# Optimization experiments

Measured on AMD Instinct MI355X. Metric: run time of the kernel, lower is better.

## Reference

```python
import jax, jax.numpy as jnp
import numpy as np

KH, KW = 3, 3  # spatial kernel from kernel_size=(1,3,3,C)


def _extract_patches_valid(x, kh, kw):
    # TF extract_image_patches ordering: depth = (row, col, channel) flattened.
    B, H, W, C = x.shape
    Ho, Wo = H - kh + 1, W - kw + 1
    # stack kh*kw shifted views -> [B, Ho, Wo, kh*kw, C]
    views = [x[:, i:i + Ho, j:j + Wo, :] for i in range(kh) for j in range(kw)]
    patches = jnp.stack(views, axis=3)
    return patches.reshape(B, Ho, Wo, kh * kw * C)


def setup_inputs() -> dict:
    key = jax.random.key(0)
    k1, k2, k3 = jax.random.split(key, 3)
    B, H, W, C = 32, 112, 112, 32
    filters = 128
    patch_dim = KH * KW * C  # 288
    x = jax.random.normal(k1, (B, H, W, C), dtype=jnp.float32)
    ccs = jax.random.uniform(k2, (patch_dim, filters), dtype=jnp.float32)  # RandomUniform(0,1)
    beta = jax.random.uniform(k3, (filters,), dtype=jnp.float32)
    return {"x": x, "ccs": ccs, "beta": beta}


def reference(x, ccs, beta):
    B = x.shape[0]
    patch_dim, filters = ccs.shape
    patches = _extract_patches_valid(x, KH, KW)  # [B, Ho, Wo, patch_dim]
    Ho, Wo = patches.shape[1], patches.shape[2]
    p = patches.reshape(B, Ho * Wo, patch_dim)  # [B, P, D]
    # squared distance: ||p||^2 - 2 p.ccs + ||ccs||^2  -> [B, P, filters]
    p_sq = jnp.sum(p * p, axis=2, keepdims=True)
    c_sq = jnp.sum(ccs * ccs, axis=0, keepdims=True)
    scores = p_sq - 2.0 * jnp.einsum('bpd,df->bpf', p, ccs) + c_sq
    out = jnp.exp(-beta * scores)  # RBF activation, beta broadcast over filters
    return out.reshape(B, Ho, Wo, filters)
```

## Files before the change

kernel.cpp:

```cpp
#include <hip/hip_runtime.h>


typedef __attribute__((ext_vector_type(8))) short bf16x8;
typedef __attribute__((ext_vector_type(4))) float f32x4;

#define HH 112
#define WW 112
#define CC 32
#define HO 110
#define WO 110
#define NF 128
#define KD 288
#define RPX 114
#define XP 32
#define ORPB 2
#define SROWS 4

__device__ __forceinline__ unsigned short f32_to_bf16(float f) {
    unsigned u = __float_as_uint(f);
    unsigned r = u + 0x7FFFu + ((u >> 16) & 1u);
    return (unsigned short)(r >> 16);
}

__global__ __launch_bounds__(256) void rbf_prologue(const float* __restrict__ ccs,
                                                    unsigned short* __restrict__ ccs_t,
                                                    float* __restrict__ c_sq) {
    int idx = blockIdx.x * 256 + threadIdx.x;
    int d = idx >> 7;
    int f = idx & 127;
    ccs_t[f * KD + d] = f32_to_bf16(ccs[idx]);
    if (blockIdx.x == 0 && threadIdx.x < 128) {
        const int fc = threadIdx.x;
        float s = 0.f;
        #pragma unroll 8
        for (int dd = 0; dd < KD; ++dd) {
            float v = ccs[dd * NF + fc];
            s += v * v;
        }
        c_sq[fc] = s;
    }
}

__global__ __launch_bounds__(256, 4) void rbf_main(const float* __restrict__ x,
                                                   const unsigned short* __restrict__ ccs_t,
                                                   const float* __restrict__ c_sq,
                                                   const float* __restrict__ beta,
                                                   float* __restrict__ out) {
    __shared__ unsigned short xs[SROWS * RPX * XP];
    __shared__ float colsum[452];
    __shared__ float p_sq[ORPB * 112];

    const int t = threadIdx.x;
    const int y0 = blockIdx.x * ORPB;
    const int b = blockIdx.y;

    #pragma unroll
    for (int p = 0; p < 14; ++p) {
        int idx = t + p * 256;
        int q = idx & 7;
        int ic = idx >> 3;
        int col = ic % 112;
        int i = ic / 112;
        const float4 v = *(const float4*)(x + ((size_t)(b * HH + y0 + i) * WW + col) * CC + q * 4);
        unsigned short h0 = f32_to_bf16(v.x), h1 = f32_to_bf16(v.y);
        unsigned short h2 = f32_to_bf16(v.z), h3 = f32_to_bf16(v.w);
        uint2 pk;
        pk.x = (unsigned)h0 | ((unsigned)h1 << 16);
        pk.y = (unsigned)h2 | ((unsigned)h3 << 16);
        *(uint2*)(&xs[(i * RPX + col) * XP + q * 4]) = pk;
        float part = v.x * v.x + v.y * v.y + v.z * v.z + v.w * v.w;
        part += __shfl_xor(part, 1);
        part += __shfl_xor(part, 2);
        part += __shfl_xor(part, 4);
        if (q == 0) colsum[ic] = part;
    }
    __syncthreads();

    if (t < ORPB * 112) {
        int r = t / 112;
        int c = t - r * 112;
        float s = 0.f;
        #pragma unroll
        for (int i = 0; i < 3; ++i)
            #pragma unroll
            for (int j = 0; j < 3; ++j)
                s += colsum[(r + i) * 112 + c + j];
        p_sq[t] = s;
    }
    __syncthreads();

    const int lane  = t & 63;
    const int wave  = t >> 6;
    const int laneM = lane & 15;
    const int quad  = lane >> 4;
    const int pl    = laneM & 1;

    const unsigned short* ap0 = ccs_t + (size_t)(wave * 32 + laneM) * KD + quad * 8;
    const unsigned short* ap1 = ap0 + 16 * KD;

    const int fb = wave * 32 + quad * 4;

    for (int r = 0; r < ORPB; ++r) {
        f32x4 acc[7][2];
        #pragma unroll
        for (int mi = 0; mi < 7; ++mi) {
            acc[mi][0] = (f32x4){0.f, 0.f, 0.f, 0.f};
            acc[mi][1] = (f32x4){0.f, 0.f, 0.f, 0.f};
        }

        #pragma unroll
        for (int kb = 0; kb < 9; ++kb) {
            const int ki = kb / 3, kj = kb % 3;
            bf16x8 a0 = *(const bf16x8*)(ap0 + kb * 32);
            bf16x8 a1 = *(const bf16x8*)(ap1 + kb * 32);
            #pragma unroll
            for (int mi = 0; mi < 7; ++mi) {
                const bf16x8 bf = *(const bf16x8*)(&xs[((r + ki) * RPX + mi * 16 + laneM + kj) * XP + quad * 8]);
                acc[mi][0] = __builtin_amdgcn_mfma_f32_16x16x32_bf16(a0, bf, acc[mi][0], 0, 0, 0);
                acc[mi][1] = __builtin_amdgcn_mfma_f32_16x16x32_bf16(a1, bf, acc[mi][1], 0, 0, 0);
            }
        }

        const float4 cs0 = *(const float4*)(c_sq + fb);
        const float4 cs1 = *(const float4*)(c_sq + fb + 16);
        const float4 bt0 = *(const float4*)(beta + fb);
        const float4 bt1 = *(const float4*)(beta + fb + 16);
        float* orow = out + (size_t)((b * HO + y0 + r) * WO) * NF;
        #pragma unroll
        for (int mi = 0; mi < 7; ++mi) {
            const int px = mi * 16 + laneM;
            const float ps = p_sq[r * 112 + px];
            f32x4 o0, o1;
            o0[0] = __expf(-bt0.x * (ps - 2.f * acc[mi][0][0] + cs0.x));
            o0[1] = __expf(-bt0.y * (ps - 2.f * acc[mi][0][1] + cs0.y));
            o0[2] = __expf(-bt0.z * (ps - 2.f * acc[mi][0][2] + cs0.z));
            o0[3] = __expf(-bt0.w * (ps - 2.f * acc[mi][0][3] + cs0.w));
            o1[0] = __expf(-bt1.x * (ps - 2.f * acc[mi][1][0] + cs1.x));
            o1[1] = __expf(-bt1.y * (ps - 2.f * acc[mi][1][1] + cs1.y));
            o1[2] = __expf(-bt1.z * (ps - 2.f * acc[mi][1][2] + cs1.z));
            o1[3] = __expf(-bt1.w * (ps - 2.f * acc[mi][1][3] + cs1.w));

            f32x4 sendv = pl ? o0 : o1;
            f32x4 recv;
            recv[0] = __shfl_xor(sendv[0], 1);
            recv[1] = __shfl_xor(sendv[1], 1);
            recv[2] = __shfl_xor(sendv[2], 1);
            recv[3] = __shfl_xor(sendv[3], 1);
            const f32x4 v1 = pl ? recv : o0;
            const f32x4 v2 = pl ? o1 : recv;

            const int pxe = mi * 16 + (laneM & ~1);
            float* op1 = orow + (size_t)pxe * NF + fb + pl * 16;
            if (pxe < WO)
                __builtin_nontemporal_store(v1, (f32x4*)op1);
            if (pxe + 1 < WO)
                __builtin_nontemporal_store(v2, (f32x4*)(op1 + NF));
        }
    }
}

extern "C" void kernel_launch(void* const* d_in, const int* in_sizes, int n_in,
                              void* d_out, int out_size, void* d_ws, size_t ws_size,
                              hipStream_t stream) {
    const float* x    = (const float*)d_in[0];
    const float* ccs  = (const float*)d_in[1];
    const float* beta = (const float*)d_in[2];
    float* out = (float*)d_out;

    unsigned short* ccs_t = (unsigned short*)d_ws;
    float* c_sq = (float*)((char*)d_ws + 128 * KD * sizeof(unsigned short));

    rbf_prologue<<<144, 256, 0, stream>>>(ccs, ccs_t, c_sq);
    rbf_main<<<dim3(55, 32), 256, 0, stream>>>(x, ccs_t, c_sq, beta, out);
}
```

Baseline: 262.3 us.

## Process eight output rows per block with rolling smem ring and prefetch

```diff
diff --git a/kernel.cpp b/kernel.cpp
--- a/kernel.cpp
+++ b/kernel.cpp
@@ -13,8 +13,8 @@
 #define KD 288
 #define RPX 114
 #define XP 32
-#define ORPB 2
-#define SROWS 4
+#define SLOTS 6
+#define CSP 116
 
 __device__ __forceinline__ unsigned short f32_to_bf16(float f) {
     unsigned u = __float_as_uint(f);
@@ -41,18 +41,25 @@
     }
 }
 
-__global__ __launch_bounds__(256, 4) void rbf_main(const float* __restrict__ x,
-                                                   const unsigned short* __restrict__ ccs_t,
-                                                   const float* __restrict__ c_sq,
-                                                   const float* __restrict__ beta,
-                                                   float* __restrict__ out) {
-    __shared__ unsigned short xs[SROWS * RPX * XP];
-    __shared__ float colsum[452];
-    __shared__ float p_sq[ORPB * 112];
+__global__ __launch_bounds__(256) void rbf_main(const float* __restrict__ x,
+                                                const unsigned short* __restrict__ ccs_t,
+                                                const float* __restrict__ c_sq,
+                                                const float* __restrict__ beta,
+                                                float* __restrict__ out) {
+    __shared__ unsigned short xs[SLOTS * RPX * XP];
+    __shared__ float colsum[SLOTS * CSP];
+    __shared__ float p_sq[2 * 112];
 
     const int t = threadIdx.x;
-    const int y0 = blockIdx.x * ORPB;
-    const int b = blockIdx.y;
+    const int y0 = blockIdx.x * 8;
+    const int b  = blockIdx.y;
+    const int ns = (HO - y0 >= 8) ? 4 : ((HO - y0) >> 1);
+
+    const int lane  = t & 63;
+    const int wave  = t >> 6;
+    const int laneM = lane & 15;
+    const int quad  = lane >> 4;
+    const int pl    = laneM & 1;
 
     #pragma unroll
     for (int p = 0; p < 14; ++p) {
@@ -72,89 +79,145 @@
         part += __shfl_xor(part, 1);
         part += __shfl_xor(part, 2);
         part += __shfl_xor(part, 4);
-        if (q == 0) colsum[ic] = part;
+        if (q == 0) colsum[i * CSP + col] = part;
     }
     __syncthreads();
 
-    if (t < ORPB * 112) {
-        int r = t / 112;
-        int c = t - r * 112;
+    if (t < 224) {
+        int r = t / 112, c = t - (t / 112) * 112;
         float s = 0.f;
         #pragma unroll
         for (int i = 0; i < 3; ++i)
             #pragma unroll
             for (int j = 0; j < 3; ++j)
-                s += colsum[(r + i) * 112 + c + j];
+                s += colsum[(r + i) * CSP + c + j];
         p_sq[t] = s;
     }
     __syncthreads();
-
-    const int lane  = t & 63;
-    const int wave  = t >> 6;
-    const int laneM = lane & 15;
-    const int quad  = lane >> 4;
-    const int pl    = laneM & 1;
 
     const unsigned short* ap0 = ccs_t + (size_t)(wave * 32 + laneM) * KD + quad * 8;
     const unsigned short* ap1 = ap0 + 16 * KD;
 
     const int fb = wave * 32 + quad * 4;
-
-    for (int r = 0; r < ORPB; ++r) {
-        f32x4 acc[7][2];
+    const float4 cs0 = *(const float4*)(c_sq + fb);
+    const float4 cs1 = *(const float4*)(c_sq + fb + 16);
+    const float4 bt0 = *(const float4*)(beta + fb);
+    const float4 bt1 = *(const float4*)(beta + fb + 16);
+
+    float4 pre[7];
+
+    for (int k = 0; k < ns; ++k) {
+        const bool more = (k < ns - 1);
+
+        if (more) {
+            #pragma unroll
+            for (int p = 0; p < 7; ++p) {
+                int idx = t + p * 256;
+                int ic = idx >> 3;
+                int q = idx & 7;
+                int col = ic % 112;
+                int i = ic / 112;
+                pre[p] = *(const float4*)(x + ((size_t)(b * HH + y0 + 2 * k + 4 + i) * WW + col) * CC + q * 4);
+            }
+        }
+
+        int sb[4];
         #pragma unroll
-        for (int mi = 0; mi < 7; ++mi) {
-            acc[mi][0] = (f32x4){0.f, 0.f, 0.f, 0.f};
-            acc[mi][1] = (f32x4){0.f, 0.f, 0.f, 0.f};
-        }
-
-        #pragma unroll
-        for (int kb = 0; kb < 9; ++kb) {
-            const int ki = kb / 3, kj = kb % 3;
-            bf16x8 a0 = *(const bf16x8*)(ap0 + kb * 32);
-            bf16x8 a1 = *(const bf16x8*)(ap1 + kb * 32);
+        for (int d = 0; d < 4; ++d) sb[d] = ((2 * k + d) % SLOTS) * RPX;
+
+        for (int r = 0; r < 2; ++r) {
+            f32x4 acc[7][2];
             #pragma unroll
             for (int mi = 0; mi < 7; ++mi) {
-                const bf16x8 bf = *(const bf16x8*)(&xs[((r + ki) * RPX + mi * 16 + laneM + kj) * XP + quad * 8]);
-                acc[mi][0] = __builtin_amdgcn_mfma_f32_16x16x32_bf16(a0, bf, acc[mi][0], 0, 0, 0);
-                acc[mi][1] = __builtin_amdgcn_mfma_f32_16x16x32_bf16(a1, bf, acc[mi][1], 0, 0, 0);
-            }
-        }
-
-        const float4 cs0 = *(const float4*)(c_sq + fb);
-        const float4 cs1 = *(const float4*)(c_sq + fb + 16);
-        const float4 bt0 = *(const float4*)(beta + fb);
-        const float4 bt1 = *(const float4*)(beta + fb + 16);
-        float* orow = out + (size_t)((b * HO + y0 + r) * WO) * NF;
-        #pragma unroll
-        for (int mi = 0; mi < 7; ++mi) {
-            const int px = mi * 16 + laneM;
-            const float ps = p_sq[r * 112 + px];
-            f32x4 o0, o1;
-            o0[0] = __expf(-bt0.x * (ps - 2.f * acc[mi][0][0] + cs0.x));
-            o0[1] = __expf(-bt0.y * (ps - 2.f * acc[mi][0][1] + cs0.y));
-            o0[2] = __expf(-bt0.z * (ps - 2.f * acc[mi][0][2] + cs0.z));
-            o0[3] = __expf(-bt0.w * (ps - 2.f * acc[mi][0][3] + cs0.w));
-            o1[0] = __expf(-bt1.x * (ps - 2.f * acc[mi][1][0] + cs1.x));
-            o1[1] = __expf(-bt1.y * (ps - 2.f * acc[mi][1][1] + cs1.y));
-            o1[2] = __expf(-bt1.z * (ps - 2.f * acc[mi][1][2] + cs1.z));
-            o1[3] = __expf(-bt1.w * (ps - 2.f * acc[mi][1][3] + cs1.w));
-
-            f32x4 sendv = pl ? o0 : o1;
-            f32x4 recv;
-            recv[0] = __shfl_xor(sendv[0], 1);
-            recv[1] = __shfl_xor(sendv[1], 1);
-            recv[2] = __shfl_xor(sendv[2], 1);
-            recv[3] = __shfl_xor(sendv[3], 1);
-            const f32x4 v1 = pl ? recv : o0;
-            const f32x4 v2 = pl ? o1 : recv;
-
-            const int pxe = mi * 16 + (laneM & ~1);
-            float* op1 = orow + (size_t)pxe * NF + fb + pl * 16;
-            if (pxe < WO)
-                __builtin_nontemporal_store(v1, (f32x4*)op1);
-            if (pxe + 1 < WO)
-                __builtin_nontemporal_store(v2, (f32x4*)(op1 + NF));
+                acc[mi][0] = (f32x4){0.f, 0.f, 0.f, 0.f};
+                acc[mi][1] = (f32x4){0.f, 0.f, 0.f, 0.f};
+            }
+
+            #pragma unroll
+            for (int kb = 0; kb < 9; ++kb) {
+                const int ki = kb / 3, kj = kb % 3;
+                bf16x8 a0 = *(const bf16x8*)(ap0 + kb * 32);
+                bf16x8 a1 = *(const bf16x8*)(ap1 + kb * 32);
+                #pragma unroll
+                for (int mi = 0; mi < 7; ++mi) {
+                    const bf16x8 bf = *(const bf16x8*)(&xs[(sb[r + ki] + mi * 16 + laneM + kj) * XP + quad * 8]);
+                    acc[mi][0] = __builtin_amdgcn_mfma_f32_16x16x32_bf16(a0, bf, acc[mi][0], 0, 0, 0);
+                    acc[mi][1] = __builtin_amdgcn_mfma_f32_16x16x32_bf16(a1, bf, acc[mi][1], 0, 0, 0);
+                }
+            }
+
+            float* orow = out + (size_t)((b * HO + y0 + 2 * k + r) * WO) * NF;
+            #pragma unroll
+            for (int mi = 0; mi < 7; ++mi) {
+                const int px = mi * 16 + laneM;
+                const float ps = p_sq[r * 112 + px];
+                f32x4 o0, o1;
+                o0[0] = __expf(-bt0.x * (ps - 2.f * acc[mi][0][0] + cs0.x));
+                o0[1] = __expf(-bt0.y * (ps - 2.f * acc[mi][0][1] + cs0.y));
+                o0[2] = __expf(-bt0.z * (ps - 2.f * acc[mi][0][2] + cs0.z));
+                o0[3] = __expf(-bt0.w * (ps - 2.f * acc[mi][0][3] + cs0.w));
+                o1[0] = __expf(-bt1.x * (ps - 2.f * acc[mi][1][0] + cs1.x));
+                o1[1] = __expf(-bt1.y * (ps - 2.f * acc[mi][1][1] + cs1.y));
+                o1[2] = __expf(-bt1.z * (ps - 2.f * acc[mi][1][2] + cs1.z));
+                o1[3] = __expf(-bt1.w * (ps - 2.f * acc[mi][1][3] + cs1.w));
+
+                f32x4 sendv = pl ? o0 : o1;
+                f32x4 recv;
+                recv[0] = __shfl_xor(sendv[0], 1);
+                recv[1] = __shfl_xor(sendv[1], 1);
+                recv[2] = __shfl_xor(sendv[2], 1);
+                recv[3] = __shfl_xor(sendv[3], 1);
+                const f32x4 v1 = pl ? recv : o0;
+                const f32x4 v2 = pl ? o1 : recv;
+
+                const int pxe = mi * 16 + (laneM & ~1);
+                float* op1 = orow + (size_t)pxe * NF + fb + pl * 16;
+                if (pxe < WO)
+                    __builtin_nontemporal_store(v1, (f32x4*)op1);
+                if (pxe + 1 < WO)
+                    __builtin_nontemporal_store(v2, (f32x4*)(op1 + NF));
+            }
+        }
+
+        if (more) {
+            __syncthreads();
+
+            #pragma unroll
+            for (int p = 0; p < 7; ++p) {
+                int idx = t + p * 256;
+                int q = idx & 7;
+                int ic = idx >> 3;
+                int col = ic % 112;
+                int i = ic / 112;
+                int sl = (2 * k + 4 + i) % SLOTS;
+                const float4 v = pre[p];
+                unsigned short h0 = f32_to_bf16(v.x), h1 = f32_to_bf16(v.y);
+                unsigned short h2 = f32_to_bf16(v.z), h3 = f32_to_bf16(v.w);
+                uint2 pk;
+                pk.x = (unsigned)h0 | ((unsigned)h1 << 16);
+                pk.y = (unsigned)h2 | ((unsigned)h3 << 16);
+                *(uint2*)(&xs[(sl * RPX + col) * XP + q * 4]) = pk;
+                float part = v.x * v.x + v.y * v.y + v.z * v.z + v.w * v.w;
+                part += __shfl_xor(part, 1);
+                part += __shfl_xor(part, 2);
+                part += __shfl_xor(part, 4);
+                if (q == 0) colsum[sl * CSP + col] = part;
+            }
+            __syncthreads();
+
+            if (t < 224) {
+                int r = t / 112, c = t - (t / 112) * 112;
+                float s = 0.f;
+                #pragma unroll
+                for (int i = 0; i < 3; ++i) {
+                    int sl = (2 * k + 2 + r + i) % SLOTS;
+                    #pragma unroll
+                    for (int j = 0; j < 3; ++j)
+                        s += colsum[sl * CSP + c + j];
+                }
+                p_sq[t] = s;
+            }
+            __syncthreads();
         }
     }
 }
@@ -171,5 +234,5 @@
     float* c_sq = (float*)((char*)d_ws + 128 * KD * sizeof(unsigned short));
 
     rbf_prologue<<<144, 256, 0, stream>>>(ccs, ccs_t, c_sq);
-    rbf_main<<<dim3(55, 32), 256, 0, stream>>>(x, ccs_t, c_sq, beta, out);
-}
+    rbf_main<<<dim3(14, 32), 256, 0, stream>>>(x, ccs_t, c_sq, beta, out);
+}
```

New measurement: 292.5 us. 1.11x slower.
